# Kernel tuning notes

Hardware: AMD Instinct MI355X
Metric: run time of the kernel (lower is better)

## Reference

```python
import jax, jax.numpy as jnp
import numpy as np

N_NODES = 10000
N_EDGES = 640000
IN_FEAT = 128
HIDDEN = 128
CLASSES = 2
NEG_SLOPE = 0.2


def glorot(key, shape):
    lim = float(np.sqrt(6.0 / (shape[0] + shape[-1])))
    return jax.random.uniform(key, shape, jnp.float32, -lim, lim)


def setup_inputs() -> dict:
    key = jax.random.key(0)
    ks = jax.random.split(key, 10)
    x = jax.random.normal(ks[0], (N_NODES, IN_FEAT), jnp.float32)
    edge_index = jax.random.randint(ks[1], (2, N_EDGES), 0, N_NODES, jnp.int64)
    return {
        "x": x,
        "edge_index": edge_index,
        "W1": glorot(ks[2], (IN_FEAT, HIDDEN)),
        "a_src1": glorot(ks[3], (HIDDEN, 1))[:, 0],
        "a_dst1": glorot(ks[4], (HIDDEN, 1))[:, 0],
        "b1": jnp.zeros((HIDDEN,), jnp.float32),
        "W2": glorot(ks[5], (HIDDEN, CLASSES)),
        "a_src2": glorot(ks[6], (CLASSES, 1))[:, 0],
        "a_dst2": glorot(ks[7], (CLASSES, 1))[:, 0],
        "b2": jnp.zeros((CLASSES,), jnp.float32),
    }


def gat_conv(x, src, dst, W, a_src, a_dst, b, n_nodes):
    # x: [N, Fin] -> h: [N, Fout]
    h = x @ W
    # per-node attention logits (single head)
    alpha_s = h @ a_src  # [N]
    alpha_d = h @ a_dst  # [N]
    e = jax.nn.leaky_relu(alpha_s[src] + alpha_d[dst], NEG_SLOPE)  # [E]
    # segment softmax over incoming edges of each dst node
    m = jax.ops.segment_max(e, dst, num_segments=n_nodes)
    ex = jnp.exp(e - m[dst])
    denom = jax.ops.segment_sum(ex, dst, num_segments=n_nodes)
    w = ex / denom[dst]  # [E]
    # weighted scatter-aggregate of source messages
    out = jax.ops.segment_sum(h[src] * w[:, None], dst, num_segments=n_nodes)
    return out + b


def reference(x, edge_index, W1, a_src1, a_dst1, b1, W2, a_src2, a_dst2, b2):
    n = x.shape[0]
    # PyG GATConv default: add self-loops
    loops = jnp.arange(n, dtype=edge_index.dtype)
    src = jnp.concatenate([edge_index[0], loops])
    dst = jnp.concatenate([edge_index[1], loops])
    h = gat_conv(x, src, dst, W1, a_src1, a_dst1, b1, n)
    h = jax.nn.relu(h)
    out = gat_conv(h, src, dst, W2, a_src2, a_dst2, b2, n)
    return out
```

## Files before the change

kernel.cpp:

```cpp
#include <hip/hip_runtime.h>
#include <hip/hip_bf16.h>

#define NN 10000
#define NE 640000
#define ETOT (NE + NN)
#define FEAT 128
#define NEG 0.2f
#define CAP 160
#define NBUCK 157
#define BCAP 5120
#define EPB 4096
#define NB1 ((ETOT + EPB - 1) / EPB)
#define GEMM_ROWS 16
#define NBG (NN / GEMM_ROWS)
#define NJOB1 (NB1 + NBG)
#define NJAGG ((NN + 3) / 4)

typedef short bf16x8 __attribute__((ext_vector_type(8)));
typedef float f32x4  __attribute__((ext_vector_type(4)));

__device__ __forceinline__ short f2bf(float f) {
    unsigned u = __float_as_uint(f);
    unsigned r = (u + 0x7FFFu + ((u >> 16) & 1u)) >> 16;
    return (short)r;
}

union ShMem {
    struct {
        int hist[160]; int scan[256]; int excl[160]; int cursor[160]; int base[160];
        unsigned int pairs[EPB];
    } p;
    struct { float rs[GEMM_ROWS][2]; float rd[GEMM_ROWS][2]; } g;
};

__device__ __forceinline__ int detect64(const void* ep) {
    const unsigned long long* p64 = (const unsigned long long*)ep;
    unsigned long long v = p64[threadIdx.x & 63];
    unsigned long long bal = __ballot((v >> 32) != 0ULL);
    return (bal == 0ULL) ? 1 : 0;
}

__global__ __launch_bounds__(256) void prep_kernel(
        const float* __restrict__ W1, const float* __restrict__ a_src1,
        const float* __restrict__ a_dst1,
        unsigned short* __restrict__ W1t, float* __restrict__ wa, float* __restrict__ wd,
        int* __restrict__ gbcnt) {
    int idx = blockIdx.x * 256 + threadIdx.x;
    if (idx < FEAT * FEAT) {
        int n = idx >> 7, k = idx & 127;
        W1t[n * FEAT + k] = (unsigned short)f2bf(W1[k * FEAT + n]);
    }
    int i2 = idx - FEAT * FEAT;
    if (i2 >= 0 && i2 < NBUCK * 16) gbcnt[i2] = 0;
    int i3 = idx - (FEAT * FEAT + NBUCK * 16);
    if (i3 >= 0 && i3 < FEAT) {
        float s = 0.f;
        for (int k = 0; k < FEAT; k++) s += W1[i3 * FEAT + k] * a_src1[k];
        wa[i3] = s;
    } else if (i3 >= FEAT && i3 < 2 * FEAT) {
        int j = i3 - FEAT;
        float s = 0.f;
        for (int k = 0; k < FEAT; k++) s += W1[j * FEAT + k] * a_dst1[k];
        wd[j] = s;
    }
}

__device__ __forceinline__ void bin_job(const void* ep, int flag64,
        int* __restrict__ gbcnt, unsigned int* __restrict__ staged,
        ShMem& sh, int tid, int job) {
    for (int i = tid; i < 160; i += 256) sh.p.hist[i] = 0;
    __syncthreads();
    const int e0 = job * EPB;
    int nE = ETOT - e0; if (nE > EPB) nE = EPB;
    const bool full = (nE == EPB);
    unsigned int key[16];
    if (full) {
#pragma unroll
        for (int k = 0; k < 16; k++) {
            int e = e0 + tid + k * 256, s, d;
            if (e < NE) {
                if (flag64) { const long long* p = (const long long*)ep; s = (int)p[e]; d = (int)p[NE + e]; }
                else        { const int* p = (const int*)ep;       s = p[e];       d = p[NE + e]; }
            } else { s = e - NE; d = s; }
            key[k] = ((unsigned)d << 14) | (unsigned)s;
            atomicAdd(&sh.p.hist[d >> 6], 1);
        }
    } else {
        for (int k = 0; k < 16; k++) {
            int idx = tid + k * 256;
            if (idx < nE) {
                int e = e0 + idx, s, d;
                if (e < NE) {
                    if (flag64) { const long long* p = (const long long*)ep; s = (int)p[e]; d = (int)p[NE + e]; }
                    else        { const int* p = (const int*)ep;       s = p[e];       d = p[NE + e]; }
                } else { s = e - NE; d = s; }
                atomicAdd(&sh.p.hist[d >> 6], 1);
            }
        }
    }
    __syncthreads();
    sh.p.scan[tid] = (tid < 160) ? sh.p.hist[tid] : 0;
    __syncthreads();
    for (int off = 1; off < 256; off <<= 1) {
        int t = (tid >= off) ? sh.p.scan[tid - off] : 0;
        __syncthreads();
        sh.p.scan[tid] += t;
        __syncthreads();
    }
    if (tid < 160) {
        int ex = sh.p.scan[tid] - sh.p.hist[tid];
        sh.p.excl[tid] = ex;
        sh.p.cursor[tid] = ex;
        sh.p.base[tid] = (tid < NBUCK && sh.p.hist[tid] > 0)
                           ? atomicAdd(&gbcnt[tid * 16], sh.p.hist[tid]) : 0;
    }
    __syncthreads();
    if (full) {
#pragma unroll
        for (int k = 0; k < 16; k++) {
            int b = key[k] >> 20;
            int pos = atomicAdd(&sh.p.cursor[b], 1);
            sh.p.pairs[pos] = key[k];
        }
    } else {
        for (int k = 0; k < 16; k++) {
            int idx = tid + k * 256;
            if (idx < nE) {
                int e = e0 + idx, s, d;
                if (e < NE) {
                    if (flag64) { const long long* p = (const long long*)ep; s = (int)p[e]; d = (int)p[NE + e]; }
                    else        { const int* p = (const int*)ep;       s = p[e];       d = p[NE + e]; }
                } else { s = e - NE; d = s; }
                unsigned int kk = ((unsigned)d << 14) | (unsigned)s;
                int pos = atomicAdd(&sh.p.cursor[d >> 6], 1);
                sh.p.pairs[pos] = kk;
            }
        }
    }
    __syncthreads();
    for (int i = tid; i < nE; i += 256) {
        unsigned int kk = sh.p.pairs[i];
        int b = kk >> 20;
        int idx = sh.p.base[b] + (i - sh.p.excl[b]);
        if (idx < BCAP) staged[b * BCAP + idx] = kk;
    }
}

__device__ __forceinline__ void gemm_job(
        const float* __restrict__ x, const unsigned short* __restrict__ W1t,
        const float* __restrict__ wa, const float* __restrict__ wd,
        unsigned short* __restrict__ h1, float* __restrict__ as1, float* __restrict__ ad1,
        ShMem& sh, int tid, int gb) {
    const int row0 = gb * GEMM_ROWS;
    const int j = tid & 127, half = tid >> 7;
    const int lane = tid & 63, wv = tid >> 6;

    float wav = wa[j], wdv = wd[j];
    int wpair = wv & 1;
    for (int rr = 0; rr < 8; rr++) {
        int r = half * 8 + rr;
        float xv = x[(size_t)(row0 + r) * FEAT + j];
        float vs = xv * wav, vd = xv * wdv;
#pragma unroll
        for (int o = 32; o; o >>= 1) { vs += __shfl_xor(vs, o); vd += __shfl_xor(vd, o); }
        if (lane == 0) { sh.g.rs[r][wpair] = vs; sh.g.rd[r][wpair] = vd; }
    }

    const int m = lane & 15, g = lane >> 4;
    const int n0 = wv * 32;
    const float* arow = x + (size_t)(row0 + m) * FEAT + g * 8;
    const unsigned short* bb0 = W1t + (size_t)(n0 + m) * FEAT + g * 8;
    const unsigned short* bb1 = W1t + (size_t)(n0 + 16 + m) * FEAT + g * 8;
    f32x4 acc0 = {0.f, 0.f, 0.f, 0.f}, acc1 = {0.f, 0.f, 0.f, 0.f};
#pragma unroll
    for (int kt = 0; kt < 4; kt++) {
        float4 v0 = *(const float4*)(arow + kt * 32);
        float4 v1 = *(const float4*)(arow + kt * 32 + 4);
        bf16x8 a;
        a[0] = f2bf(v0.x); a[1] = f2bf(v0.y); a[2] = f2bf(v0.z); a[3] = f2bf(v0.w);
        a[4] = f2bf(v1.x); a[5] = f2bf(v1.y); a[6] = f2bf(v1.z); a[7] = f2bf(v1.w);
        bf16x8 b0 = *(const bf16x8*)(bb0 + kt * 32);
        bf16x8 b1 = *(const bf16x8*)(bb1 + kt * 32);
        acc0 = __builtin_amdgcn_mfma_f32_16x16x32_bf16(a, b0, acc0, 0, 0, 0);
        acc1 = __builtin_amdgcn_mfma_f32_16x16x32_bf16(a, b1, acc1, 0, 0, 0);
    }
#pragma unroll
    for (int r = 0; r < 4; r++) {
        int row = row0 + g * 4 + r;
        h1[(size_t)row * FEAT + n0 + m]      = (unsigned short)f2bf(acc0[r]);
        h1[(size_t)row * FEAT + n0 + 16 + m] = (unsigned short)f2bf(acc1[r]);
    }
    __syncthreads();
    if (tid < GEMM_ROWS) {
        int row = row0 + tid;
        as1[row] = sh.g.rs[tid][0] + sh.g.rs[tid][1];
        ad1[row] = sh.g.rd[tid][0] + sh.g.rd[tid][1];
    }
}

__global__ __launch_bounds__(256) void fat1_kernel(const void* ep,
        const float* __restrict__ x, const unsigned short* __restrict__ W1t,
        const float* __restrict__ wa, const float* __restrict__ wd,
        int* __restrict__ gbcnt, unsigned int* __restrict__ staged,
        unsigned short* __restrict__ h1, float* __restrict__ as1, float* __restrict__ ad1) {
    __shared__ ShMem sh;
    int blk = blockIdx.x, tid = threadIdx.x;
    if (blk < NB1) { int f = detect64(ep); bin_job(ep, f, gbcnt, staged, sh, tid, blk); }
    else gemm_job(x, W1t, wa, wd, h1, as1, ad1, sh, tid, blk - NB1);
}

__global__ __launch_bounds__(1024) void scatter2_kernel(const int* __restrict__ gbcnt,
        const unsigned int* __restrict__ staged, const float* __restrict__ as1,
        const float* __restrict__ ad1, float2* __restrict__ slots2,
        int* __restrict__ deg, float* __restrict__ dsum_g) {
    __shared__ int   ncnt[64];
    __shared__ float dsum_s[64];
    __shared__ float adl[64];
    int b = blockIdx.x, tid = threadIdx.x;
    if (tid < 64) {
        ncnt[tid] = 0; dsum_s[tid] = 0.f;
        int node = b * 64 + tid;
        adl[tid] = (node < NN) ? ad1[node] : 0.f;
    }
    __syncthreads();
    int total = gbcnt[b * 16]; if (total > BCAP) total = BCAP;
    for (int i = tid; i < total; i += 1024) {
        unsigned int kk = staged[b * BCAP + i];
        int d = kk >> 14, s = kk & 0x3FFF;
        float t = as1[s] + adl[d & 63];
        t = (t > 0.f) ? t : NEG * t;
        float w = __expf(fminf(t, 80.f));
        int lp = atomicAdd(&ncnt[d & 63], 1);
        atomicAdd(&dsum_s[d & 63], w);
        if (lp < CAP) slots2[d * CAP + lp] = make_float2(w, __int_as_float(s));
    }
    __syncthreads();
    if (tid < 64) {
        int node = b * 64 + tid;
        if (node < NN) {
            deg[node] = min(ncnt[tid], CAP);
            dsum_g[node] = dsum_s[tid];
        }
    }
}

__global__ __launch_bounds__(256) void agg1_kernel(const int* __restrict__ deg,
        const float2* __restrict__ slots2, const float* __restrict__ dsum_g,
        const unsigned int* __restrict__ h1u,
        const float* __restrict__ b1, const float* __restrict__ W2,
        const float* __restrict__ a_src2, const float* __restrict__ a_dst2,
        float* __restrict__ h2, float* __restrict__ as2, float* __restrict__ ad2) {
    __shared__ float2 ws_s[4][CAP];
    int tid = threadIdx.x;
    int wi = tid >> 6, lane = tid & 63;
    int v = blockIdx.x * 4 + wi;
    if (v >= NN) return;
    int c = deg[v];
    float dsum = dsum_g[v];
    const int base = v * CAP;

    if (lane < c)       ws_s[wi][lane]       = slots2[base + lane];
    if (lane + 64 < c)  ws_s[wi][lane + 64]  = slots2[base + lane + 64];
    if (lane + 128 < c) ws_s[wi][lane + 128] = slots2[base + lane + 128];

    float ax = 0.f, ay = 0.f;
#pragma unroll 4
    for (int i = 0; i < c; i++) {
        float2 ws = ws_s[wi][i];
        float wgt = ws.x;
        int s = __float_as_int(ws.y);
        unsigned int u = h1u[s * 64 + lane];
        ax += wgt * __uint_as_float(u << 16);
        ay += wgt * __uint_as_float(u & 0xFFFF0000u);
    }
    float inv = 1.f / dsum;
    float2 bb = ((const float2*)b1)[lane];
    float hx = fmaxf(ax * inv + bb.x, 0.f);
    float hy = fmaxf(ay * inv + bb.y, 0.f);

    const float2* w2p = (const float2*)W2;
    float2 wc0 = w2p[2 * lane], wc1 = w2p[2 * lane + 1];
    float c0 = hx * wc0.x + hy * wc1.x;
    float c1 = hx * wc0.y + hy * wc1.y;
#pragma unroll
    for (int o = 32; o; o >>= 1) { c0 += __shfl_down(c0, o); c1 += __shfl_down(c1, o); }
    if (lane == 0) {
        ((float2*)h2)[v] = make_float2(c0, c1);
        as2[v] = c0 * a_src2[0] + c1 * a_src2[1];
        ad2[v] = c0 * a_dst2[0] + c1 * a_dst2[1];
    }
}

__global__ __launch_bounds__(256) void agg2_kernel(const int* __restrict__ deg,
        const float2* __restrict__ slots2, const float* __restrict__ as2,
        const float* __restrict__ ad2, const float* __restrict__ h2,
        const float* __restrict__ b2, float* __restrict__ out) {
    int tid = threadIdx.x;
    int wi = tid >> 6, lane = tid & 63;
    int v = blockIdx.x * 4 + wi;
    if (v >= NN) return;
    int c = deg[v];
    int base = v * CAP;
    float adv = ad2[v];
    float dsum = 0.f, a0 = 0.f, a1 = 0.f;
    for (int i = lane; i < c; i += 64) {
        int s = __float_as_int(slots2[base + i].y);
        float e = as2[s] + adv;
        e = (e > 0.f) ? e : NEG * e;
        float w = __expf(fminf(e, 80.f));
        dsum += w;
        float2 hv = ((const float2*)h2)[s];
        a0 += w * hv.x; a1 += w * hv.y;
    }
#pragma unroll
    for (int o = 32; o; o >>= 1) {
        dsum += __shfl_xor(dsum, o);
        a0 += __shfl_xor(a0, o);
        a1 += __shfl_xor(a1, o);
    }
    if (lane == 0) {
        out[v * 2]     = a0 / dsum + b2[0];
        out[v * 2 + 1] = a1 / dsum + b2[1];
    }
}

extern "C" void kernel_launch(void* const* d_in, const int* in_sizes, int n_in,
                              void* d_out, int out_size, void* d_ws, size_t ws_size,
                              hipStream_t stream) {
    const float* x      = (const float*)d_in[0];
    const void*  edges  = d_in[1];
    const float* W1     = (const float*)d_in[2];
    const float* a_src1 = (const float*)d_in[3];
    const float* a_dst1 = (const float*)d_in[4];
    const float* b1     = (const float*)d_in[5];
    const float* W2     = (const float*)d_in[6];
    const float* a_src2 = (const float*)d_in[7];
    const float* a_dst2 = (const float*)d_in[8];
    const float* b2     = (const float*)d_in[9];
    float* out = (float*)d_out;

    char* w = (char*)d_ws;
    size_t off = 0;
    auto alloc = [&](size_t bytes) { void* p = w + off; off += (bytes + 255) & ~size_t(255); return p; };
    int*             gbcnt  = (int*)alloc((size_t)NBUCK * 16 * 4);
    unsigned int*    staged = (unsigned int*)alloc((size_t)NBUCK * BCAP * 4);
    float2*          slots2 = (float2*)alloc((size_t)NN * CAP * 8);
    int*             deg    = (int*)alloc((size_t)NN * 4);
    float*           dsum_g = (float*)alloc((size_t)NN * 4);
    unsigned short*  h1     = (unsigned short*)alloc((size_t)NN * FEAT * 2);
    unsigned short*  W1t    = (unsigned short*)alloc((size_t)FEAT * FEAT * 2);
    float*           wa     = (float*)alloc(FEAT * 4);
    float*           wd     = (float*)alloc(FEAT * 4);
    float*           as1    = (float*)alloc(NN * 4);
    float*           ad1    = (float*)alloc(NN * 4);
    float*           h2     = (float*)alloc(NN * 2 * 4);
    float*           as2    = (float*)alloc(NN * 4);
    float*           ad2    = (float*)alloc(NN * 4);

    int prep_items = FEAT * FEAT + NBUCK * 16 + 2 * FEAT;
    prep_kernel<<<(prep_items + 255) / 256, 256, 0, stream>>>(W1, a_src1, a_dst1,
                                                              W1t, wa, wd, gbcnt);
    fat1_kernel<<<NJOB1, 256, 0, stream>>>(edges, x, W1t, wa, wd,
                                           gbcnt, staged, h1, as1, ad1);
    scatter2_kernel<<<NBUCK, 1024, 0, stream>>>(gbcnt, staged, as1, ad1,
                                                slots2, deg, dsum_g);
    agg1_kernel<<<NJAGG, 256, 0, stream>>>(deg, slots2, dsum_g,
                                           (const unsigned int*)h1, b1,
                                           W2, a_src2, a_dst2, h2, as2, ad2);
    agg2_kernel<<<NJAGG, 256, 0, stream>>>(deg, slots2, as2, ad2, h2, b2, out);
}
```

Baseline: 60.98 us.

## Fuse bucket scatter with layer-1 aggregation using shared-memory edge lists

Merges the scatter and layer-1 aggregation kernels into one. Each 1024-thread block builds per-destination edge lists in shared memory, packing a bf16 weight with the source index into 32 bits, then aggregates four nodes per wave. It also writes a packed slot array, half the size of the old one, for the layer-2 kernel. This removes a launch and the global round trip of the float2 slot array. In exchange, only 157 blocks run the heavy gather, which lowers parallelism, and the edge weights drop to bf16 precision.

```diff
diff --git a/kernel.cpp b/kernel.cpp
--- a/kernel.cpp
+++ b/kernel.cpp
@@ -209,10 +209,14 @@
     else gemm_job(x, W1t, wa, wd, h1, as1, ad1, sh, tid, blk - NB1);
 }
 
-__global__ __launch_bounds__(1024) void scatter2_kernel(const int* __restrict__ gbcnt,
+__global__ __launch_bounds__(1024) void scatagg1_kernel(const int* __restrict__ gbcnt,
         const unsigned int* __restrict__ staged, const float* __restrict__ as1,
-        const float* __restrict__ ad1, float2* __restrict__ slots2,
-        int* __restrict__ deg, float* __restrict__ dsum_g) {
+        const float* __restrict__ ad1, const unsigned int* __restrict__ h1u,
+        const float* __restrict__ b1, const float* __restrict__ W2,
+        const float* __restrict__ a_src2, const float* __restrict__ a_dst2,
+        unsigned int* __restrict__ slotsP, int* __restrict__ deg,
+        float* __restrict__ h2, float* __restrict__ as2, float* __restrict__ ad2) {
+    __shared__ unsigned int lists[64][CAP];
     __shared__ int   ncnt[64];
     __shared__ float dsum_s[64];
     __shared__ float adl[64];
@@ -223,6 +227,7 @@
         adl[tid] = (node < NN) ? ad1[node] : 0.f;
     }
     __syncthreads();
+
     int total = gbcnt[b * 16]; if (total > BCAP) total = BCAP;
     for (int i = tid; i < total; i += 1024) {
         unsigned int kk = staged[b * BCAP + i];
@@ -232,67 +237,61 @@
         float w = __expf(fminf(t, 80.f));
         int lp = atomicAdd(&ncnt[d & 63], 1);
         atomicAdd(&dsum_s[d & 63], w);
-        if (lp < CAP) slots2[d * CAP + lp] = make_float2(w, __int_as_float(s));
-    }
-    __syncthreads();
-    if (tid < 64) {
-        int node = b * 64 + tid;
-        if (node < NN) {
-            deg[node] = min(ncnt[tid], CAP);
-            dsum_g[node] = dsum_s[tid];
-        }
-    }
-}
-
-__global__ __launch_bounds__(256) void agg1_kernel(const int* __restrict__ deg,
-        const float2* __restrict__ slots2, const float* __restrict__ dsum_g,
-        const unsigned int* __restrict__ h1u,
-        const float* __restrict__ b1, const float* __restrict__ W2,
-        const float* __restrict__ a_src2, const float* __restrict__ a_dst2,
-        float* __restrict__ h2, float* __restrict__ as2, float* __restrict__ ad2) {
-    __shared__ float2 ws_s[4][CAP];
-    int tid = threadIdx.x;
-    int wi = tid >> 6, lane = tid & 63;
-    int v = blockIdx.x * 4 + wi;
-    if (v >= NN) return;
-    int c = deg[v];
-    float dsum = dsum_g[v];
-    const int base = v * CAP;
-
-    if (lane < c)       ws_s[wi][lane]       = slots2[base + lane];
-    if (lane + 64 < c)  ws_s[wi][lane + 64]  = slots2[base + lane + 64];
-    if (lane + 128 < c) ws_s[wi][lane + 128] = slots2[base + lane + 128];
-
-    float ax = 0.f, ay = 0.f;
-#pragma unroll 4
-    for (int i = 0; i < c; i++) {
-        float2 ws = ws_s[wi][i];
-        float wgt = ws.x;
-        int s = __float_as_int(ws.y);
-        unsigned int u = h1u[s * 64 + lane];
-        ax += wgt * __uint_as_float(u << 16);
-        ay += wgt * __uint_as_float(u & 0xFFFF0000u);
-    }
-    float inv = 1.f / dsum;
+        if (lp < CAP)
+            lists[d & 63][lp] = ((unsigned)(unsigned short)f2bf(w) << 16) | (unsigned)s;
+    }
+    __syncthreads();
+
+    int wv = tid >> 6, lane = tid & 63;
+    int nl[4], vv[4], cc[4];
+    float ax[4] = {0,0,0,0}, ay[4] = {0,0,0,0};
+    int cmax = 0;
+#pragma unroll
+    for (int nn = 0; nn < 4; nn++) {
+        nl[nn] = wv * 4 + nn;
+        vv[nn] = b * 64 + nl[nn];
+        cc[nn] = (vv[nn] < NN) ? min(ncnt[nl[nn]], CAP) : 0;
+        cmax = max(cmax, cc[nn]);
+    }
+    for (int i = 0; i < cmax; i++) {
+#pragma unroll
+        for (int nn = 0; nn < 4; nn++) {
+            if (i < cc[nn]) {
+                unsigned int u = lists[nl[nn]][i];
+                float wgt = __uint_as_float(u & 0xFFFF0000u);
+                int s = u & 0x3FFF;
+                unsigned int hv = h1u[s * 64 + lane];
+                ax[nn] += wgt * __uint_as_float(hv << 16);
+                ay[nn] += wgt * __uint_as_float(hv & 0xFFFF0000u);
+            }
+        }
+    }
     float2 bb = ((const float2*)b1)[lane];
-    float hx = fmaxf(ax * inv + bb.x, 0.f);
-    float hy = fmaxf(ay * inv + bb.y, 0.f);
-
     const float2* w2p = (const float2*)W2;
     float2 wc0 = w2p[2 * lane], wc1 = w2p[2 * lane + 1];
-    float c0 = hx * wc0.x + hy * wc1.x;
-    float c1 = hx * wc0.y + hy * wc1.y;
-#pragma unroll
-    for (int o = 32; o; o >>= 1) { c0 += __shfl_down(c0, o); c1 += __shfl_down(c1, o); }
-    if (lane == 0) {
-        ((float2*)h2)[v] = make_float2(c0, c1);
-        as2[v] = c0 * a_src2[0] + c1 * a_src2[1];
-        ad2[v] = c0 * a_dst2[0] + c1 * a_dst2[1];
+#pragma unroll
+    for (int nn = 0; nn < 4; nn++) {
+        if (vv[nn] >= NN) continue;
+        float inv = 1.f / dsum_s[nl[nn]];
+        float hx = fmaxf(ax[nn] * inv + bb.x, 0.f);
+        float hy = fmaxf(ay[nn] * inv + bb.y, 0.f);
+        float c0 = hx * wc0.x + hy * wc1.x;
+        float c1 = hx * wc0.y + hy * wc1.y;
+#pragma unroll
+        for (int o = 32; o; o >>= 1) { c0 += __shfl_down(c0, o); c1 += __shfl_down(c1, o); }
+        if (lane == 0) {
+            ((float2*)h2)[vv[nn]] = make_float2(c0, c1);
+            as2[vv[nn]] = c0 * a_src2[0] + c1 * a_src2[1];
+            ad2[vv[nn]] = c0 * a_dst2[0] + c1 * a_dst2[1];
+            deg[vv[nn]] = cc[nn];
+        }
+        for (int i = lane; i < cc[nn]; i += 64)
+            slotsP[(size_t)vv[nn] * CAP + i] = lists[nl[nn]][i];
     }
 }
 
 __global__ __launch_bounds__(256) void agg2_kernel(const int* __restrict__ deg,
-        const float2* __restrict__ slots2, const float* __restrict__ as2,
+        const unsigned int* __restrict__ slotsP, const float* __restrict__ as2,
         const float* __restrict__ ad2, const float* __restrict__ h2,
         const float* __restrict__ b2, float* __restrict__ out) {
     int tid = threadIdx.x;
@@ -300,11 +299,11 @@
     int v = blockIdx.x * 4 + wi;
     if (v >= NN) return;
     int c = deg[v];
-    int base = v * CAP;
+    size_t base = (size_t)v * CAP;
     float adv = ad2[v];
     float dsum = 0.f, a0 = 0.f, a1 = 0.f;
     for (int i = lane; i < c; i += 64) {
-        int s = __float_as_int(slots2[base + i].y);
+        int s = slotsP[base + i] & 0x3FFF;
         float e = as2[s] + adv;
         e = (e > 0.f) ? e : NEG * e;
         float w = __expf(fminf(e, 80.f));
@@ -344,9 +343,8 @@
     auto alloc = [&](size_t bytes) { void* p = w + off; off += (bytes + 255) & ~size_t(255); return p; };
     int*             gbcnt  = (int*)alloc((size_t)NBUCK * 16 * 4);
     unsigned int*    staged = (unsigned int*)alloc((size_t)NBUCK * BCAP * 4);
-    float2*          slots2 = (float2*)alloc((size_t)NN * CAP * 8);
+    unsigned int*    slotsP = (unsigned int*)alloc((size_t)NN * CAP * 4);
     int*             deg    = (int*)alloc((size_t)NN * 4);
-    float*           dsum_g = (float*)alloc((size_t)NN * 4);
     unsigned short*  h1     = (unsigned short*)alloc((size_t)NN * FEAT * 2);
     unsigned short*  W1t    = (unsigned short*)alloc((size_t)FEAT * FEAT * 2);
     float*           wa     = (float*)alloc(FEAT * 4);
@@ -362,10 +360,9 @@
                                                               W1t, wa, wd, gbcnt);
     fat1_kernel<<<NJOB1, 256, 0, stream>>>(edges, x, W1t, wa, wd,
                                            gbcnt, staged, h1, as1, ad1);
-    scatter2_kernel<<<NBUCK, 1024, 0, stream>>>(gbcnt, staged, as1, ad1,
-                                                slots2, deg, dsum_g);
-    agg1_kernel<<<NJAGG, 256, 0, stream>>>(deg, slots2, dsum_g,
-                                           (const unsigned int*)h1, b1,
-                                           W2, a_src2, a_dst2, h2, as2, ad2);
-    agg2_kernel<<<NJAGG, 256, 0, stream>>>(deg, slots2, as2, ad2, h2, b2, out);
-}
+    scatagg1_kernel<<<NBUCK, 1024, 0, stream>>>(gbcnt, staged, as1, ad1,
+                                                (const unsigned int*)h1, b1,
+                                                W2, a_src2, a_dst2,
+                                                slotsP, deg, h2, as2, ad2);
+    agg2_kernel<<<NJAGG, 256, 0, stream>>>(deg, slotsP, as2, ad2, h2, b2, out);
+}
```

After: 111.1 us. 1.82x slower.
